# Kernel optimization log

Hardware: AMD Instinct MI355X
Metric: run time of the kernel (lower is better)

The kernel has to match this reference:

```python
import jax, jax.numpy as jnp
import numpy as np

B, T, D, H = 4, 2048, 1024, 16
HD = D // H
EPS = 1e-5


def gelu_tanh(x):
    c = jnp.sqrt(jnp.asarray(2.0 / jnp.pi, x.dtype))
    return 0.5 * x * (1.0 + jnp.tanh(c * (x + 0.044715 * x * x * x)))


def layernorm(x, gamma, beta):
    mean = jnp.mean(x, axis=-1, keepdims=True)
    var = jnp.var(x, axis=-1, keepdims=True)
    return gamma * (x - mean) / jnp.sqrt(var + EPS) + beta


def setup_inputs() -> dict:
    key = jax.random.key(0)
    ks = jax.random.split(key, 12)
    s = 0.02
    return {
        "x": jax.random.normal(ks[0], (B, T, D), jnp.float32),
        "Wq": jax.random.normal(ks[1], (D, D), jnp.float32) * s,
        "Wk": jax.random.normal(ks[2], (D, D), jnp.float32) * s,
        "Wv": jax.random.normal(ks[3], (D, D), jnp.float32) * s,
        "Wo": jax.random.normal(ks[4], (D, D), jnp.float32) * s,
        "bo": jnp.zeros((D,), jnp.float32),
        "W1": jax.random.normal(ks[5], (D, 4 * D), jnp.float32) * s,
        "b1": jnp.zeros((4 * D,), jnp.float32),
        "W2": jax.random.normal(ks[6], (4 * D, D), jnp.float32) * s,
        "b2": jnp.zeros((D,), jnp.float32),
        "gamma1": jnp.ones((D,), jnp.float32),
        "beta1": jnp.zeros((D,), jnp.float32),
        "gamma2": jnp.ones((D,), jnp.float32),
        "beta2": jnp.zeros((D,), jnp.float32),
    }


def reference(x, Wq, Wk, Wv, Wo, bo, W1, b1, W2, b2, gamma1, beta1, gamma2, beta2):
    # --- attention sublayer (pre-norm, causal) ---
    h = layernorm(x, gamma1, beta1)
    q = (h @ Wq).reshape(B, T, H, HD).transpose(0, 2, 1, 3)  # (B,H,T,hd)
    k = (h @ Wk).reshape(B, T, H, HD).transpose(0, 2, 1, 3)
    v = (h @ Wv).reshape(B, T, H, HD).transpose(0, 2, 1, 3)
    scores = jnp.einsum("bhqd,bhkd->bhqk", q, k) * (HD ** -0.5)
    causal = jnp.tril(jnp.ones((T, T), bool))
    scores = jnp.where(causal, scores, -jnp.inf)
    w = jax.nn.softmax(scores, axis=-1)
    attn = jnp.einsum("bhqk,bhkd->bhqd", w, v).transpose(0, 2, 1, 3).reshape(B, T, D)
    x = x + (attn @ Wo + bo)
    # --- FFN sublayer ---
    h2 = layernorm(x, gamma2, beta2)
    ff = gelu_tanh(h2 @ W1 + b1) @ W2 + b2
    return x + ff
```

## Files before the change

### kernel.cpp

```cpp
#include <hip/hip_runtime.h>
#include <hip/hip_bf16.h>


typedef __bf16 bf16;
typedef __attribute__((ext_vector_type(8))) __bf16 bf16x8;
typedef __attribute__((ext_vector_type(4))) __bf16 bf16x4;
typedef __attribute__((ext_vector_type(4))) float floatx4;

#define EXPC 0.18033688011112042f

__device__ __forceinline__ void async_cp16(const bf16* g, bf16* l) {
  __builtin_amdgcn_global_load_lds(
      (const __attribute__((address_space(1))) void*)g,
      (__attribute__((address_space(3))) void*)l, 16, 0, 0);
}

__global__ __launch_bounds__(256) void transpose_cvt4(
    const float* __restrict__ S0, const float* __restrict__ S1,
    const float* __restrict__ S2, const float* __restrict__ S3,
    bf16* __restrict__ D0, bf16* __restrict__ D1, bf16* __restrict__ D2,
    bf16* __restrict__ D3, int K, int N) {
  const float* W = (blockIdx.z == 0) ? S0 : (blockIdx.z == 1) ? S1
                   : (blockIdx.z == 2) ? S2 : S3;
  bf16* WT = (blockIdx.z == 0) ? D0 : (blockIdx.z == 1) ? D1
             : (blockIdx.z == 2) ? D2 : D3;
  __shared__ bf16 tile[32][33];
  const int tn = blockIdx.x;
  const int tk = blockIdx.y;
  const int t = threadIdx.x;
  const int row = t >> 3;
  const int c4 = (t & 7) * 4;

  const float* src = W + (size_t)(tk * 32 + row) * N + tn * 32 + c4;
  float4 v = *(const float4*)src;
  tile[row][c4 + 0] = (bf16)v.x;
  tile[row][c4 + 1] = (bf16)v.y;
  tile[row][c4 + 2] = (bf16)v.z;
  tile[row][c4 + 3] = (bf16)v.w;
  __syncthreads();
  bf16x4 o;
  o[0] = tile[c4 + 0][row];
  o[1] = tile[c4 + 1][row];
  o[2] = tile[c4 + 2][row];
  o[3] = tile[c4 + 3][row];
  *(bf16x4*)(WT + (size_t)(tn * 32 + row) * K + tk * 32 + c4) = o;
}

__global__ __launch_bounds__(256) void transpose_cvt(
    const float* __restrict__ W, bf16* __restrict__ WT, int K, int N) {
  __shared__ bf16 tile[32][33];
  const int tn = blockIdx.x;
  const int tk = blockIdx.y;
  const int t = threadIdx.x;
  const int row = t >> 3;
  const int c4 = (t & 7) * 4;

  const float* src = W + (size_t)(tk * 32 + row) * N + tn * 32 + c4;
  float4 v = *(const float4*)src;
  tile[row][c4 + 0] = (bf16)v.x;
  tile[row][c4 + 1] = (bf16)v.y;
  tile[row][c4 + 2] = (bf16)v.z;
  tile[row][c4 + 3] = (bf16)v.w;
  __syncthreads();
  bf16x4 o;
  o[0] = tile[c4 + 0][row];
  o[1] = tile[c4 + 1][row];
  o[2] = tile[c4 + 2][row];
  o[3] = tile[c4 + 3][row];
  *(bf16x4*)(WT + (size_t)(tn * 32 + row) * K + tk * 32 + c4) = o;
}

__global__ __launch_bounds__(256) void vtrans_kernel(
    const bf16* __restrict__ QKV, bf16* __restrict__ Vt) {
  const int tt = blockIdx.x;
  const int bh = blockIdx.y;
  const int b = bh >> 4, h = bh & 15;
  __shared__ bf16 tile[64][72];
  const int t = threadIdx.x;
  const int row = t >> 3;
  const int c8 = (t & 7) * 8;
  const size_t vbase = (size_t)b * 2048 * 3072 + 2048 + (size_t)h * 64;
  const bf16* src = QKV + vbase + (size_t)(tt * 64 + row) * 3072 + c8;
  *(bf16x8*)&tile[row][c8] = *(const bf16x8*)src;
  *(bf16x8*)&tile[row + 32][c8] = *(const bf16x8*)(src + (size_t)32 * 3072);
  __syncthreads();
  bf16x8 o0, o1;
#pragma unroll
  for (int j = 0; j < 8; ++j) {
    o0[j] = tile[c8 + j][row];
    o1[j] = tile[c8 + j][row + 32];
  }
  bf16* dst = Vt + ((size_t)bh * 64 + row) * 2048 + tt * 64 + c8;
  *(bf16x8*)dst = o0;
  *(bf16x8*)(dst + (size_t)32 * 2048) = o1;
}

__global__ __launch_bounds__(256) void ln_kernel(
    const float* __restrict__ x, const float* __restrict__ gamma,
    const float* __restrict__ beta, bf16* __restrict__ out) {
  const int row = blockIdx.x;
  const int t = threadIdx.x;
  const float* xr = x + (size_t)row * 1024;
  float4 v4 = *(const float4*)(xr + t * 4);
  float a[4] = {v4.x, v4.y, v4.z, v4.w};
  float s = a[0] + a[1] + a[2] + a[3];
  float ss = a[0] * a[0] + a[1] * a[1] + a[2] * a[2] + a[3] * a[3];
  for (int off = 1; off < 64; off <<= 1) {
    s += __shfl_xor(s, off);
    ss += __shfl_xor(ss, off);
  }
  __shared__ float red[8];
  const int wid = t >> 6, lane = t & 63;
  if (lane == 0) { red[wid] = s; red[wid + 4] = ss; }
  __syncthreads();
  s = red[0] + red[1] + red[2] + red[3];
  ss = red[4] + red[5] + red[6] + red[7];
  const float mean = s * (1.0f / 1024.0f);
  const float var = ss * (1.0f / 1024.0f) - mean * mean;
  const float rstd = rsqrtf(var + 1e-5f);
  bf16x4 o;
  for (int j = 0; j < 4; ++j) {
    float g = gamma[t * 4 + j];
    float b = beta[t * 4 + j];
    o[j] = (bf16)((a[j] - mean) * rstd * g + b);
  }
  *(bf16x4*)(out + (size_t)row * 1024 + t * 4) = o;
}

__device__ __forceinline__ float gelu_f(float x) {
  const float c = 0.7978845608028654f;
  float u = c * (x + 0.044715f * x * x * x);
  u = fminf(fmaxf(u, -10.0f), 10.0f);
  float t = __builtin_exp2f(u * 2.8853900817779268f);
  return x * t * __builtin_amdgcn_rcpf(t + 1.0f);
}

template <int MODE, int BK>
__global__ __launch_bounds__(256, 2) void gemm_bt(
    const bf16* __restrict__ A, const bf16* __restrict__ BT,
    const float* __restrict__ bias, const float* __restrict__ resid,
    void* __restrict__ out, int M, int N, int K) {
  __shared__ bf16 sA[128 * BK];
  __shared__ bf16 sB[128 * BK];
  constexpr int GPR = BK / 8;
  constexpr int CPT = GPR / 2;
  constexpr int RPI = 256 / GPR;
  constexpr int SW = (BK >= 64) ? 7 : 0;

  const int t = threadIdx.x;
  const int lane = t & 63, wid = t >> 6;
  const int waveM = wid >> 1, waveN = wid & 1;
  const int quad = lane >> 4, l16 = lane & 15;
  const size_t m0 = (size_t)blockIdx.x * 128;
  const size_t n0 = (size_t)blockIdx.y * 128;

  floatx4 acc[4][4] = {};

  const int r0 = t / GPR;
  const int gp = t % GPR;
  const int gsrc = gp ^ (r0 & SW);
  const bf16* Ag = A + (m0 + r0) * (size_t)K + gsrc * 8;
  const bf16* Bg = BT + (n0 + r0) * (size_t)K + gsrc * 8;
  bf16* sAp = sA + t * 8;
  bf16* sBp = sB + t * 8;

  for (int k0 = 0; k0 < K; k0 += BK) {
    __syncthreads();
#pragma unroll
    for (int it = 0; it < CPT; ++it) {
      async_cp16(Ag + k0 + (size_t)(it * RPI) * K, sAp + it * 2048);
      async_cp16(Bg + k0 + (size_t)(it * RPI) * K, sBp + it * 2048);
    }
    __syncthreads();
#pragma unroll
    for (int ks = 0; ks < BK / 32; ++ks) {
      bf16x8 af[4], bfv[4];
#pragma unroll
      for (int i = 0; i < 4; ++i) {
        const int rowA = waveM * 64 + i * 16 + l16;
        const int g = ((ks * 4 + quad) ^ (l16 & SW)) * 8;
        af[i] = *(const bf16x8*)&sA[rowA * BK + g];
        const int rowB = waveN * 64 + i * 16 + l16;
        bfv[i] = *(const bf16x8*)&sB[rowB * BK + g];
      }
#pragma unroll
      for (int mt = 0; mt < 4; ++mt)
#pragma unroll
        for (int nt = 0; nt < 4; ++nt)
          acc[mt][nt] = __builtin_amdgcn_mfma_f32_16x16x32_bf16(
              af[mt], bfv[nt], acc[mt][nt], 0, 0, 0);
    }
  }

#pragma unroll
  for (int mt = 0; mt < 4; ++mt) {
#pragma unroll
    for (int nt = 0; nt < 4; ++nt) {
      const size_t row_base = m0 + waveM * 64 + mt * 16 + quad * 4;
      const size_t col = n0 + waveN * 64 + nt * 16 + l16;
#pragma unroll
      for (int r = 0; r < 4; ++r) {
        const size_t row = row_base + r;
        float v = acc[mt][nt][r];
        if (MODE == 1) {
          v = gelu_f(v + bias[col]);
          ((bf16*)out)[row * N + col] = (bf16)v;
        } else if (MODE == 2) {
          v += bias[col] + resid[row * N + col];
          ((float*)out)[row * N + col] = v;
        } else {
          ((bf16*)out)[row * N + col] = (bf16)v;
        }
      }
    }
  }
}

__global__ __launch_bounds__(256) void attn_kernel(
    const bf16* __restrict__ QKV, const bf16* __restrict__ Vt,
    bf16* __restrict__ O) {
  const int idx = blockIdx.x;
  const int qt = 15 - (idx >> 6);
  const int bh = idx & 63;
  const int b = bh >> 4, h = bh & 15;
  const int t = threadIdx.x;
  const int lane = t & 63, wid = t >> 6;
  const int quad = lane >> 4, l16 = lane & 15;

  __shared__ bf16 sQ[128 * 64];
  __shared__ bf16 sK[64 * 64];
  __shared__ bf16 sV[64 * 64];
  __shared__ bf16 sP[4][16][72];

  const size_t qkvbase = (size_t)b * 2048 * 3072 + (size_t)h * 64;
  const int q0 = qt * 128;

  const int r0 = t >> 3;
  const int gp = t & 7;
  const int gsw = gp ^ (r0 & 7);

  {
    const bf16* pQ = QKV + qkvbase + (size_t)(q0 + r0) * 3072 + gsw * 8;
#pragma unroll
    for (int j = 0; j < 4; ++j)
      async_cp16(pQ + (size_t)(j * 32) * 3072, sQ + j * 2048 + t * 8);
  }

  const bf16* pK = QKV + qkvbase + 1024 + (size_t)r0 * 3072 + gsw * 8;
  const bf16* pV = Vt + ((size_t)bh * 64 + r0) * 2048 + gsw * 8;
  const ptrdiff_t bumpK = (ptrdiff_t)64 * 3072;

  __syncthreads();

  bf16x8 aq[2][2];
#pragma unroll
  for (int mt = 0; mt < 2; ++mt) {
    const int row = wid * 32 + mt * 16 + l16;
#pragma unroll
    for (int ks = 0; ks < 2; ++ks)
      aq[mt][ks] =
          *(const bf16x8*)&sQ[row * 64 + (((ks * 4 + quad) ^ (row & 7)) * 8)];
  }

  float l_part[2] = {0.f, 0.f};
  floatx4 o_acc[2][4] = {};

  const int ktmax = 2 * qt + 1;
  for (int kt = 0; kt <= ktmax; ++kt) {
    __syncthreads();
    async_cp16(pK, sK + t * 8);
    async_cp16(pK + (size_t)32 * 3072, sK + 2048 + t * 8);
    async_cp16(pV, sV + t * 8);
    async_cp16(pV + (size_t)32 * 2048, sV + 2048 + t * 8);
    pK += bumpK;
    pV += 64;
    __syncthreads();

    bf16x8 bv[4][2];
#pragma unroll
    for (int nt = 0; nt < 4; ++nt) {
      const int d = nt * 16 + l16;
#pragma unroll
      for (int ks = 0; ks < 2; ++ks)
        bv[nt][ks] =
            *(const bf16x8*)&sV[d * 64 + (((ks * 4 + quad) ^ (d & 7)) * 8)];
    }

    float p[2][4][4];
#pragma unroll
    for (int nt = 0; nt < 4; ++nt) {
      const int kr = nt * 16 + l16;
      bf16x8 bk0 = *(const bf16x8*)&sK[kr * 64 + ((quad ^ (kr & 7)) * 8)];
      bf16x8 bk1 = *(const bf16x8*)&sK[kr * 64 + (((4 + quad) ^ (kr & 7)) * 8)];
#pragma unroll
      for (int mt = 0; mt < 2; ++mt) {
        floatx4 acc = {};
        acc = __builtin_amdgcn_mfma_f32_16x16x32_bf16(bk0, aq[mt][0], acc, 0, 0, 0);
        acc = __builtin_amdgcn_mfma_f32_16x16x32_bf16(bk1, aq[mt][1], acc, 0, 0, 0);
#pragma unroll
        for (int r = 0; r < 4; ++r)
          p[mt][nt][r] = __builtin_exp2f(acc[r] * EXPC);
      }
    }

    if (kt >= ktmax - 1) {
      const int k0 = kt * 64;
#pragma unroll
      for (int mt = 0; mt < 2; ++mt) {
        const int qg = q0 + wid * 32 + mt * 16 + l16;
#pragma unroll
        for (int nt = 0; nt < 4; ++nt) {
          const int kg = k0 + nt * 16 + quad * 4;
#pragma unroll
          for (int r = 0; r < 4; ++r)
            if (kg + r > qg) p[mt][nt][r] = 0.f;
        }
      }
    }

#pragma unroll
    for (int mt = 0; mt < 2; ++mt) {
#pragma unroll
      for (int nt = 0; nt < 4; ++nt) {
        bf16x4 pk;
#pragma unroll
        for (int r = 0; r < 4; ++r) {
          l_part[mt] += p[mt][nt][r];
          pk[r] = (bf16)p[mt][nt][r];
        }
        *(bf16x4*)&sP[wid][l16][nt * 16 + quad * 4] = pk;
      }
      bf16x8 ap0 = *(const bf16x8*)&sP[wid][l16][quad * 8];
      bf16x8 ap1 = *(const bf16x8*)&sP[wid][l16][32 + quad * 8];
#pragma unroll
      for (int nt = 0; nt < 4; ++nt) {
        o_acc[mt][nt] = __builtin_amdgcn_mfma_f32_16x16x32_bf16(
            ap0, bv[nt][0], o_acc[mt][nt], 0, 0, 0);
        o_acc[mt][nt] = __builtin_amdgcn_mfma_f32_16x16x32_bf16(
            ap1, bv[nt][1], o_acc[mt][nt], 0, 0, 0);
      }
    }
  }

#pragma unroll
  for (int mt = 0; mt < 2; ++mt) {
    float lt = l_part[mt];
    lt += __shfl_xor(lt, 16);
    lt += __shfl_xor(lt, 32);
    float inv[4];
#pragma unroll
    for (int r = 0; r < 4; ++r)
      inv[r] = 1.0f / __shfl(lt, quad * 4 + r);
#pragma unroll
    for (int nt = 0; nt < 4; ++nt)
#pragma unroll
      for (int r = 0; r < 4; ++r) {
        const size_t row =
            (size_t)b * 2048 + q0 + wid * 32 + mt * 16 + quad * 4 + r;
        const size_t col = (size_t)h * 64 + nt * 16 + l16;
        O[row * 1024 + col] = (bf16)(o_acc[mt][nt][r] * inv[r]);
      }
  }
}

extern "C" void kernel_launch(void* const* d_in, const int* in_sizes, int n_in,
                              void* d_out, int out_size, void* d_ws, size_t ws_size,
                              hipStream_t stream) {
  const float* x = (const float*)d_in[0];
  const float* Wq = (const float*)d_in[1];
  const float* Wk = (const float*)d_in[2];
  const float* Wv = (const float*)d_in[3];
  const float* Wo = (const float*)d_in[4];
  const float* bo = (const float*)d_in[5];
  const float* W1 = (const float*)d_in[6];
  const float* b1 = (const float*)d_in[7];
  const float* W2 = (const float*)d_in[8];
  const float* b2 = (const float*)d_in[9];
  const float* gamma1 = (const float*)d_in[10];
  const float* beta1 = (const float*)d_in[11];
  const float* gamma2 = (const float*)d_in[12];
  const float* beta2 = (const float*)d_in[13];

  char* ws = (char*)d_ws;
  const size_t MB = (size_t)1 << 20;
  bf16* WqkvT = (bf16*)(ws + 0 * MB);
  bf16* WoT = (bf16*)(ws + 6 * MB);
  bf16* W1T = (bf16*)(ws + 8 * MB);
  bf16* W2T = (bf16*)(ws + 16 * MB);
  bf16* h1  = (bf16*)(ws + 24 * MB);
  bf16* Vt  = (bf16*)(ws + 24 * MB);
  bf16* QKVb = (bf16*)(ws + 40 * MB);
  bf16* attnb = (bf16*)(ws + 88 * MB);
  float* x1 = (float*)(ws + 104 * MB);
  bf16* h2  = (bf16*)(ws + 136 * MB);
  bf16* midb = (bf16*)(ws + 152 * MB);

  dim3 blk(256);

  transpose_cvt4<<<dim3(32, 32, 4), blk, 0, stream>>>(
      Wq, Wk, Wv, Wo, WqkvT, WqkvT + (size_t)1024 * 1024,
      WqkvT + (size_t)2048 * 1024, WoT, 1024, 1024);
  transpose_cvt<<<dim3(128, 32), blk, 0, stream>>>(W1, W1T, 1024, 4096);
  transpose_cvt<<<dim3(32, 128), blk, 0, stream>>>(W2, W2T, 4096, 1024);

  ln_kernel<<<8192, blk, 0, stream>>>(x, gamma1, beta1, h1);

  gemm_bt<3, 64><<<dim3(64, 24), blk, 0, stream>>>(h1, WqkvT, nullptr, nullptr,
                                                   QKVb, 8192, 3072, 1024);

  vtrans_kernel<<<dim3(32, 64), blk, 0, stream>>>(QKVb, Vt);

  attn_kernel<<<dim3(1024), blk, 0, stream>>>(QKVb, Vt, attnb);

  gemm_bt<2, 128><<<dim3(64, 8), blk, 0, stream>>>(attnb, WoT, bo, x, x1,
                                                   8192, 1024, 1024);

  ln_kernel<<<8192, blk, 0, stream>>>(x1, gamma2, beta2, h2);

  gemm_bt<1, 64><<<dim3(64, 32), blk, 0, stream>>>(h2, W1T, b1, nullptr, midb,
                                                   8192, 4096, 1024);

  gemm_bt<2, 128><<<dim3(64, 8), blk, 0, stream>>>(midb, W2T, b2, x1, d_out,
                                                   8192, 1024, 4096);
}
```

Before: 476.3 us.

## Add 256x256 tile 8-wave GEMM with interleaved prefetch for QKV and FFN1

Adds a new GEMM kernel with 256x256 output tiles and 512 threads. It uses a double-buffered LDS pipeline with swizzled async global-to-LDS loads, splits each k-step into four MFMA phases that interleave LDS fragment reads and the next-tile prefetch, raises wave priority during MFMA bursts, and remaps workgroup IDs for cache locality. The QKV projection and the first FFN GEMM are switched to it to improve data reuse and overlap memory with compute. Larger tiles produce fewer blocks (384 and 512), which may hurt load balance, and register pressure rises with 32 accumulators per thread.

```diff
diff --git a/kernel.cpp b/kernel.cpp
--- a/kernel.cpp
+++ b/kernel.cpp
@@ -8,6 +8,7 @@
 typedef __attribute__((ext_vector_type(4))) float floatx4;
 
 #define EXPC 0.18033688011112042f
+#define MFMA16(a, b, c) __builtin_amdgcn_mfma_f32_16x16x32_bf16(a, b, c, 0, 0, 0)
 
 __device__ __forceinline__ void async_cp16(const bf16* g, bf16* l) {
   __builtin_amdgcn_global_load_lds(
@@ -202,6 +203,185 @@
       for (int r = 0; r < 4; ++r) {
         const size_t row = row_base + r;
         float v = acc[mt][nt][r];
+        if (MODE == 1) {
+          v = gelu_f(v + bias[col]);
+          ((bf16*)out)[row * N + col] = (bf16)v;
+        } else if (MODE == 2) {
+          v += bias[col] + resid[row * N + col];
+          ((float*)out)[row * N + col] = v;
+        } else {
+          ((bf16*)out)[row * N + col] = (bf16)v;
+        }
+      }
+    }
+  }
+}
+
+template <int MODE>
+__global__ __launch_bounds__(512, 2) void gemm256(
+    const bf16* __restrict__ A, const bf16* __restrict__ BT,
+    const float* __restrict__ bias, const float* __restrict__ resid,
+    void* __restrict__ out, int M, int N, int K) {
+  __shared__ bf16 sA[2][256 * 64];
+  __shared__ bf16 sB[2][256 * 64];
+
+  const int t = threadIdx.x;
+  const int lane = t & 63;
+  const int wid = t >> 6;
+  const int wm = wid >> 2;
+  const int wn = wid & 3;
+  const int quad = lane >> 4, l16 = lane & 15;
+
+  const int gx = gridDim.x;
+  int wg = blockIdx.y * gx + blockIdx.x;
+  {
+    const int nwg = gx * gridDim.y;
+    if ((nwg & 7) == 0) wg = (wg & 7) * (nwg >> 3) + (wg >> 3);
+  }
+  const size_t m0 = (size_t)(wg % gx) * 256;
+  const size_t n0 = (size_t)(wg / gx) * 256;
+
+  const int r0 = t >> 3;
+  const int gp = t & 7;
+  const int gsw = gp ^ (r0 & 7);
+  const bf16* Ag = A + (m0 + r0) * (size_t)K + gsw * 8;
+  const bf16* Bg = BT + (n0 + r0) * (size_t)K + gsw * 8;
+
+  auto stageA = [&](int d, int kt, int h) {
+    async_cp16(Ag + (size_t)(h * 128) * K + kt * 64,
+               &sA[d][(h * 128) * 64 + t * 8]);
+    async_cp16(Ag + (size_t)(h * 128 + 64) * K + kt * 64,
+               &sA[d][(h * 128 + 64) * 64 + t * 8]);
+  };
+  auto stageB = [&](int d, int kt, int h) {
+    async_cp16(Bg + (size_t)(h * 128) * K + kt * 64,
+               &sB[d][(h * 128) * 64 + t * 8]);
+    async_cp16(Bg + (size_t)(h * 128 + 64) * K + kt * 64,
+               &sB[d][(h * 128 + 64) * 64 + t * 8]);
+  };
+
+  const int NT = K >> 6;
+
+  stageA(0, 0, 0); stageA(0, 0, 1); stageB(0, 0, 0); stageB(0, 0, 1);
+  stageA(1, 1, 0); stageA(1, 1, 1); stageB(1, 1, 0); stageB(1, 1, 1);
+  asm volatile("s_waitcnt vmcnt(8)" ::: "memory");
+  __builtin_amdgcn_sched_barrier(0);
+  __builtin_amdgcn_s_barrier();
+
+  floatx4 acc[8][4] = {};
+  bf16x8 afv[4][2], bfv[4][2];
+
+  for (int kt = 0; kt < NT; ++kt) {
+    const int d = kt & 1;
+    const bf16* sAd = sA[d];
+    const bf16* sBd = sB[d];
+    const bool pf = (kt + 2 < NT);
+
+#pragma unroll
+    for (int mf = 0; mf < 4; ++mf) {
+      const int row = wm * 128 + mf * 16 + l16;
+#pragma unroll
+      for (int ks = 0; ks < 2; ++ks)
+        afv[mf][ks] = *(const bf16x8*)
+            &sAd[row * 64 + (((ks * 4 + quad) ^ (row & 7)) << 3)];
+    }
+#pragma unroll
+    for (int nf = 0; nf < 2; ++nf) {
+      const int col = wn * 64 + nf * 16 + l16;
+#pragma unroll
+      for (int ks = 0; ks < 2; ++ks)
+        bfv[nf][ks] = *(const bf16x8*)
+            &sBd[col * 64 + (((ks * 4 + quad) ^ (col & 7)) << 3)];
+    }
+    __builtin_amdgcn_s_barrier();
+    asm volatile("s_waitcnt lgkmcnt(0)" ::: "memory");
+    __builtin_amdgcn_sched_barrier(0);
+    __builtin_amdgcn_s_setprio(1);
+#pragma unroll
+    for (int mf = 0; mf < 4; ++mf)
+#pragma unroll
+      for (int nf = 0; nf < 2; ++nf) {
+        acc[mf][nf] = MFMA16(afv[mf][0], bfv[nf][0], acc[mf][nf]);
+        acc[mf][nf] = MFMA16(afv[mf][1], bfv[nf][1], acc[mf][nf]);
+      }
+    __builtin_amdgcn_s_setprio(0);
+    __builtin_amdgcn_s_barrier();
+
+#pragma unroll
+    for (int nf = 2; nf < 4; ++nf) {
+      const int col = wn * 64 + nf * 16 + l16;
+#pragma unroll
+      for (int ks = 0; ks < 2; ++ks)
+        bfv[nf][ks] = *(const bf16x8*)
+            &sBd[col * 64 + (((ks * 4 + quad) ^ (col & 7)) << 3)];
+    }
+    __builtin_amdgcn_s_barrier();
+    asm volatile("s_waitcnt lgkmcnt(0)" ::: "memory");
+    __builtin_amdgcn_sched_barrier(0);
+    __builtin_amdgcn_s_setprio(1);
+#pragma unroll
+    for (int mf = 0; mf < 4; ++mf)
+#pragma unroll
+      for (int nf = 2; nf < 4; ++nf) {
+        acc[mf][nf] = MFMA16(afv[mf][0], bfv[nf][0], acc[mf][nf]);
+        acc[mf][nf] = MFMA16(afv[mf][1], bfv[nf][1], acc[mf][nf]);
+      }
+    __builtin_amdgcn_s_setprio(0);
+    __builtin_amdgcn_s_barrier();
+
+#pragma unroll
+    for (int mf = 0; mf < 4; ++mf) {
+      const int row = wm * 128 + 64 + mf * 16 + l16;
+#pragma unroll
+      for (int ks = 0; ks < 2; ++ks)
+        afv[mf][ks] = *(const bf16x8*)
+            &sAd[row * 64 + (((ks * 4 + quad) ^ (row & 7)) << 3)];
+    }
+    if (pf) { stageB(d, kt + 2, 0); stageB(d, kt + 2, 1); }
+    __builtin_amdgcn_s_barrier();
+    asm volatile("s_waitcnt lgkmcnt(0)" ::: "memory");
+    __builtin_amdgcn_sched_barrier(0);
+    __builtin_amdgcn_s_setprio(1);
+#pragma unroll
+    for (int mf = 0; mf < 4; ++mf)
+#pragma unroll
+      for (int nf = 0; nf < 2; ++nf) {
+        acc[4 + mf][nf] = MFMA16(afv[mf][0], bfv[nf][0], acc[4 + mf][nf]);
+        acc[4 + mf][nf] = MFMA16(afv[mf][1], bfv[nf][1], acc[4 + mf][nf]);
+      }
+    __builtin_amdgcn_s_setprio(0);
+    __builtin_amdgcn_s_barrier();
+
+    if (pf) { stageA(d, kt + 2, 0); stageA(d, kt + 2, 1); }
+    __builtin_amdgcn_s_barrier();
+    __builtin_amdgcn_s_setprio(1);
+#pragma unroll
+    for (int mf = 0; mf < 4; ++mf)
+#pragma unroll
+      for (int nf = 2; nf < 4; ++nf) {
+        acc[4 + mf][nf] = MFMA16(afv[mf][0], bfv[nf][0], acc[4 + mf][nf]);
+        acc[4 + mf][nf] = MFMA16(afv[mf][1], bfv[nf][1], acc[4 + mf][nf]);
+      }
+    __builtin_amdgcn_s_setprio(0);
+    if (pf) {
+      asm volatile("s_waitcnt vmcnt(8)" ::: "memory");
+    } else if (kt + 1 < NT) {
+      asm volatile("s_waitcnt vmcnt(0)" ::: "memory");
+    }
+    __builtin_amdgcn_sched_barrier(0);
+    __builtin_amdgcn_s_barrier();
+  }
+
+#pragma unroll
+  for (int mf = 0; mf < 8; ++mf) {
+#pragma unroll
+    for (int nf = 0; nf < 4; ++nf) {
+      const size_t row_base = m0 + wm * 128 + mf * 16 + quad * 4;
+      const size_t col = n0 + wn * 64 + nf * 16 + l16;
+#pragma unroll
+      for (int r = 0; r < 4; ++r) {
+        const size_t row = row_base + r;
+        float v = acc[mf][nf][r];
         if (MODE == 1) {
           v = gelu_f(v + bias[col]);
           ((bf16*)out)[row * N + col] = (bf16)v;
@@ -405,8 +585,8 @@
 
   ln_kernel<<<8192, blk, 0, stream>>>(x, gamma1, beta1, h1);
 
-  gemm_bt<3, 64><<<dim3(64, 24), blk, 0, stream>>>(h1, WqkvT, nullptr, nullptr,
-                                                   QKVb, 8192, 3072, 1024);
+  gemm256<3><<<dim3(32, 12), dim3(512), 0, stream>>>(
+      h1, WqkvT, nullptr, nullptr, QKVb, 8192, 3072, 1024);
 
   vtrans_kernel<<<dim3(32, 64), blk, 0, stream>>>(QKVb, Vt);
 
@@ -417,8 +597,8 @@
 
   ln_kernel<<<8192, blk, 0, stream>>>(x1, gamma2, beta2, h2);
 
-  gemm_bt<1, 64><<<dim3(64, 32), blk, 0, stream>>>(h2, W1T, b1, nullptr, midb,
-                                                   8192, 4096, 1024);
+  gemm256<1><<<dim3(32, 16), dim3(512), 0, stream>>>(
+      h2, W1T, b1, nullptr, midb, 8192, 4096, 1024);
 
   gemm_bt<2, 128><<<dim3(64, 8), blk, 0, stream>>>(midb, W2T, b2, x1, d_out,
                                                    8192, 1024, 4096);
```

Result: no change. 482.0 us (+1.2%).

## Prefetch next K/V tile into LDS while computing current attention tile

Applied to the files above, without the earlier changes.

The attention loop now issues the first K/V async copy before the loop. Each iteration loads all K and V fragments from LDS into registers, then hits a barrier and issues the async global-to-LDS copy for the next tile, so that copy runs during the QK MFMA, softmax and PV work. This removes the exposed global load latency at the top of each iteration. In exchange it uses more registers for the K fragments and relies on hand-placed waitcnt and s_barrier ordering for correctness.

```diff
diff --git a/kernel.cpp b/kernel.cpp
--- a/kernel.cpp
+++ b/kernel.cpp
@@ -250,6 +250,13 @@
   const bf16* pV = Vt + ((size_t)bh * 64 + r0) * 2048 + gsw * 8;
   const ptrdiff_t bumpK = (ptrdiff_t)64 * 3072;
 
+  async_cp16(pK, sK + t * 8);
+  async_cp16(pK + (size_t)32 * 3072, sK + 2048 + t * 8);
+  async_cp16(pV, sV + t * 8);
+  async_cp16(pV + (size_t)32 * 2048, sV + 2048 + t * 8);
+  pK += bumpK;
+  pV += 64;
+
   __syncthreads();
 
   bf16x8 aq[2][2];
@@ -267,16 +274,13 @@
 
   const int ktmax = 2 * qt + 1;
   for (int kt = 0; kt <= ktmax; ++kt) {
-    __syncthreads();
-    async_cp16(pK, sK + t * 8);
-    async_cp16(pK + (size_t)32 * 3072, sK + 2048 + t * 8);
-    async_cp16(pV, sV + t * 8);
-    async_cp16(pV + (size_t)32 * 2048, sV + 2048 + t * 8);
-    pK += bumpK;
-    pV += 64;
-    __syncthreads();
-
-    bf16x8 bv[4][2];
+    if (kt) {
+      asm volatile("s_waitcnt vmcnt(0)" ::: "memory");
+      __builtin_amdgcn_sched_barrier(0);
+      __builtin_amdgcn_s_barrier();
+    }
+
+    bf16x8 bv[4][2], bkf[4][2];
 #pragma unroll
     for (int nt = 0; nt < 4; ++nt) {
       const int d = nt * 16 + l16;
@@ -284,19 +288,33 @@
       for (int ks = 0; ks < 2; ++ks)
         bv[nt][ks] =
             *(const bf16x8*)&sV[d * 64 + (((ks * 4 + quad) ^ (d & 7)) * 8)];
+      const int kr = nt * 16 + l16;
+      bkf[nt][0] = *(const bf16x8*)&sK[kr * 64 + ((quad ^ (kr & 7)) * 8)];
+      bkf[nt][1] = *(const bf16x8*)&sK[kr * 64 + (((4 + quad) ^ (kr & 7)) * 8)];
+    }
+    asm volatile("s_waitcnt lgkmcnt(0)" ::: "memory");
+    __builtin_amdgcn_sched_barrier(0);
+    __builtin_amdgcn_s_barrier();
+
+    if (kt < ktmax) {
+      async_cp16(pK, sK + t * 8);
+      async_cp16(pK + (size_t)32 * 3072, sK + 2048 + t * 8);
+      async_cp16(pV, sV + t * 8);
+      async_cp16(pV + (size_t)32 * 2048, sV + 2048 + t * 8);
+      pK += bumpK;
+      pV += 64;
     }
 
     float p[2][4][4];
 #pragma unroll
     for (int nt = 0; nt < 4; ++nt) {
-      const int kr = nt * 16 + l16;
-      bf16x8 bk0 = *(const bf16x8*)&sK[kr * 64 + ((quad ^ (kr & 7)) * 8)];
-      bf16x8 bk1 = *(const bf16x8*)&sK[kr * 64 + (((4 + quad) ^ (kr & 7)) * 8)];
 #pragma unroll
       for (int mt = 0; mt < 2; ++mt) {
         floatx4 acc = {};
-        acc = __builtin_amdgcn_mfma_f32_16x16x32_bf16(bk0, aq[mt][0], acc, 0, 0, 0);
-        acc = __builtin_amdgcn_mfma_f32_16x16x32_bf16(bk1, aq[mt][1], acc, 0, 0, 0);
+        acc = __builtin_amdgcn_mfma_f32_16x16x32_bf16(bkf[nt][0], aq[mt][0],
+                                                      acc, 0, 0, 0);
+        acc = __builtin_amdgcn_mfma_f32_16x16x32_bf16(bkf[nt][1], aq[mt][1],
+                                                      acc, 0, 0, 0);
 #pragma unroll
         for (int r = 0; r < 4; ++r)
           p[mt][nt][r] = __builtin_exp2f(acc[r] * EXPC);
```

New measurement: 479.8 us. Within noise of the previous version (+0.7%).
